# Optimization experiments

Hardware: AMD Instinct MI355X
Metric: run time of the kernel (lower is better)

## Reference

```python
import jax, jax.numpy as jnp
import numpy as np

STU, EXER, KNOW, D = 100000, 50000, 123, 64
N_NODES = STU + EXER
N_EDGES = 1200000
GCN_LAYERS = 3


def setup_inputs() -> dict:
    key = jax.random.key(0)
    ks = jax.random.split(key, 10)
    return {
        "student_id": jax.random.randint(ks[0], (8192,), 0, STU, dtype=jnp.int64) if jax.config.jax_enable_x64 else jax.random.randint(ks[0], (8192,), 0, STU, dtype=jnp.int32),
        "exercise_id": jax.random.randint(ks[1], (8192,), 0, EXER, dtype=jnp.int32),
        "q_mask": jax.random.randint(ks[2], (8192, KNOW), 0, 2, dtype=jnp.int32),
        "edge_row": jax.random.randint(ks[3], (N_EDGES,), 0, N_NODES, dtype=jnp.int32),
        "edge_col": jax.random.randint(ks[4], (N_EDGES,), 0, N_NODES, dtype=jnp.int32),
        "edge_val": jax.random.uniform(ks[5], (N_EDGES,), dtype=jnp.float32),
        # learned parameters (xavier-normal-ish init)
        "stu_emb": jax.random.normal(ks[6], (STU, D), dtype=jnp.float32) * 0.02,
        "exer_emb": jax.random.normal(ks[7], (EXER, D), dtype=jnp.float32) * 0.02,
        "disc_emb": jax.random.normal(ks[8], (EXER, 1), dtype=jnp.float32) * 0.02,
        "know_emb": jax.random.normal(ks[9], (KNOW, D), dtype=jnp.float32) * 0.02,
    }


def reference(student_id, exercise_id, q_mask, edge_row, edge_col, edge_val,
              stu_emb, exer_emb, disc_emb, know_emb):
    # LightGCN propagation (eval path: no edge dropout, matching self.training=False)
    s = stu_emb.shape[0]
    all_emb = jnp.concatenate([stu_emb, exer_emb], axis=0)  # [N, D]
    acc = all_emb
    h = all_emb
    for _ in range(GCN_LAYERS):
        # SpMM: out[r] = sum_e val[e] * h[col[e]] for edges with row[e]==r
        msgs = edge_val[:, None] * h[edge_col]               # [E, D]
        h = jax.ops.segment_sum(msgs, edge_row, num_segments=N_NODES)
        acc = acc + h
    light_out = acc / jnp.asarray(GCN_LAYERS + 1, dtype=acc.dtype)  # mean over layer stack
    stus = light_out[:s]
    exers = light_out[s:]
    student_ts = stus[student_id]        # [B, D]
    diff_ts = exers[exercise_id]         # [B, D]
    disc_ts = disc_emb[exercise_id]      # [B, 1]
    knowledge_ts = know_emb              # [K, D]
    return (student_ts, diff_ts, disc_ts, knowledge_ts)
```

## Files before the change

### kernel.cpp

```cpp
#include <hip/hip_runtime.h>


#define STU 100000
#define EXER 50000
#define KNOW 123
#define DIM 64
#define N_NODES 150000
#define N_EDGES 1200000
#define NB 8192
#define BR 256
#define NBUCK 586
#define PB 256
#define EPB 4688
#define NSB 586
#define SCAP 3072

typedef unsigned short bfu;

__device__ __forceinline__ bfu f2bf(float f) {
    unsigned int u = __float_as_uint(f);
    unsigned int r = (u + 0x7FFFu + ((u >> 16) & 1u)) >> 16;
    return (bfu)r;
}
__device__ __forceinline__ float bf2f(bfu h) {
    return __uint_as_float((unsigned int)h << 16);
}

__global__ void k_conv0(const float* __restrict__ stu, const float* __restrict__ exer,
                        bfu* __restrict__ b0) {
    long long i = (long long)blockIdx.x * blockDim.x + threadIdx.x;
    long long n4 = ((long long)N_NODES * DIM) >> 2;
    if (i >= n4) return;
    long long stu4 = ((long long)STU * DIM) >> 2;
    float4 v = (i < stu4) ? ((const float4*)stu)[i]
                          : ((const float4*)exer)[i - stu4];
    ushort4 o;
    o.x = f2bf(v.x); o.y = f2bf(v.y); o.z = f2bf(v.z); o.w = f2bf(v.w);
    ((ushort4*)b0)[i] = o;
}

__global__ __launch_bounds__(1024) void k_count(const int* __restrict__ erow,
                                                int* __restrict__ gcounts) {
    __shared__ int cnt[NBUCK];
    for (int i = threadIdx.x; i < NBUCK; i += 1024) cnt[i] = 0;
    __syncthreads();
    int b = blockIdx.x;
    long long s = (long long)b * EPB;
    long long e = s + EPB; if (e > N_EDGES) e = N_EDGES;
    for (long long k = s + threadIdx.x; k < e; k += 1024)
        atomicAdd(&cnt[__builtin_nontemporal_load(&erow[k]) >> 8], 1);
    __syncthreads();
    for (int i = threadIdx.x; i < NBUCK; i += 1024) gcounts[i * PB + b] = cnt[i];
}

__global__ void k_scan1(const int* __restrict__ gin, int* __restrict__ gout,
                        int* __restrict__ bsum) {
    __shared__ int s[256];
    int i = blockIdx.x * 256 + threadIdx.x;
    int v = gin[i];
    s[threadIdx.x] = v;
    __syncthreads();
    for (int o = 1; o < 256; o <<= 1) {
        int x = (threadIdx.x >= o) ? s[threadIdx.x - o] : 0;
        __syncthreads();
        s[threadIdx.x] += x;
        __syncthreads();
    }
    gout[i] = s[threadIdx.x] - v;
    if (threadIdx.x == 255) bsum[blockIdx.x] = s[255];
}

__global__ void k_scan2(const int* __restrict__ bsum, int* __restrict__ bsumoff) {
    __shared__ int s[1024];
    int t = threadIdx.x;
    int v = (t < NSB) ? bsum[t] : 0;
    s[t] = v;
    __syncthreads();
    for (int o = 1; o < 1024; o <<= 1) {
        int x = (t >= o) ? s[t - o] : 0;
        __syncthreads();
        s[t] += x;
        __syncthreads();
    }
    if (t < NSB) bsumoff[t] = s[t] - v;
}

__global__ void k_scan3(int* __restrict__ gout, const int* __restrict__ bsumoff,
                        int* __restrict__ boff) {
    int i = blockIdx.x * 256 + threadIdx.x;
    int v = gout[i] + bsumoff[i >> 8];
    gout[i] = v;
    if ((i & 255) == 0) boff[i >> 8] = v;
    if (i == 0) boff[NBUCK] = N_EDGES;
}

__global__ __launch_bounds__(1024) void k_place(const int* __restrict__ erow,
                                                const int* __restrict__ ecol,
                                                const float* __restrict__ eval,
                                                const int* __restrict__ gscan,
                                                int2* __restrict__ bedge) {
    __shared__ int2 staged[EPB];
    __shared__ unsigned short sbkt[EPB];
    __shared__ int lbase[NBUCK];
    __shared__ int lcur[NBUCK];
    __shared__ int gbase[NBUCK];
    __shared__ int stmp[1024];
    int b = blockIdx.x, tid = threadIdx.x;
    for (int i = tid; i < NBUCK; i += 1024) lcur[i] = 0;
    __syncthreads();
    long long s = (long long)b * EPB;
    long long e = s + EPB; if (e > N_EDGES) e = N_EDGES;
    int n = (int)(e - s);
    for (int k = tid; k < n; k += 1024)
        atomicAdd(&lcur[__builtin_nontemporal_load(&erow[s + k]) >> 8], 1);
    __syncthreads();
    int v = (tid < NBUCK) ? lcur[tid] : 0;
    stmp[tid] = v;
    __syncthreads();
    for (int o = 1; o < 1024; o <<= 1) {
        int x = (tid >= o) ? stmp[tid - o] : 0;
        __syncthreads();
        stmp[tid] += x;
        __syncthreads();
    }
    if (tid < NBUCK) { lbase[tid] = stmp[tid] - v; lcur[tid] = stmp[tid] - v; }
    for (int i = tid; i < NBUCK; i += 1024) gbase[i] = gscan[i * PB + b];
    __syncthreads();
    for (int k = tid; k < n; k += 1024) {
        int r = __builtin_nontemporal_load(&erow[s + k]);
        int c = __builtin_nontemporal_load(&ecol[s + k]);
        float vv = __builtin_nontemporal_load(&eval[s + k]);
        int bk = r >> 8;
        int p = atomicAdd(&lcur[bk], 1);
        staged[p] = make_int2((r & 255) | (c << 8), __float_as_int(vv));
        sbkt[p] = (unsigned short)bk;
    }
    __syncthreads();
    for (int t = tid; t < n; t += 1024) {
        int bk = sbkt[t];
        bedge[gbase[bk] + (t - lbase[bk])] = staged[t];
    }
}

__global__ __launch_bounds__(512) void k_sort(const int* __restrict__ boff,
                                              const int2* __restrict__ bedge,
                                              int2* __restrict__ sedge,
                                              int* __restrict__ off) {
    __shared__ int2 st[SCAP];
    __shared__ int2 st2[SCAP];
    __shared__ int hist[BR];
    __shared__ int cur[BR];
    __shared__ int stmp[512];
    int b = blockIdx.x, tid = threadIdx.x;
    int s = boff[b], e = boff[b + 1];
    int n = e - s; if (n > SCAP) n = SCAP;
    for (int i = tid; i < BR; i += 512) hist[i] = 0;
    __syncthreads();
    for (int t = tid; t < n; t += 512) {
        int2 ev = bedge[s + t];
        st[t] = ev;
        atomicAdd(&hist[ev.x & 255], 1);
    }
    __syncthreads();
    int v = (tid < BR) ? hist[tid] : 0;
    stmp[tid] = v;
    __syncthreads();
    for (int o = 1; o < 512; o <<= 1) {
        int x = (tid >= o) ? stmp[tid - o] : 0;
        __syncthreads();
        stmp[tid] += x;
        __syncthreads();
    }
    if (tid < BR) {
        int ex = stmp[tid] - v;
        cur[tid] = ex;
        off[b * BR + tid] = s + ex;
    }
    __syncthreads();
    for (int t = tid; t < n; t += 512) {
        int2 ev = st[t];
        int p = atomicAdd(&cur[ev.x & 255], 1);
        st2[p] = make_int2((unsigned)ev.x >> 8, ev.y);
    }
    __syncthreads();
    for (int t = tid; t < n; t += 512) sedge[s + t] = st2[t];
}

__global__ void k_gather2(const int* __restrict__ off, const int2* __restrict__ sedge,
                          const bfu* __restrict__ h, bfu* __restrict__ out) {
    int w = (blockIdx.x * blockDim.x + threadIdx.x) >> 6;
    if (w >= N_NODES / 2) return;
    int lane = threadIdx.x & 63;
    int half = lane >> 5, l32 = lane & 31;
    int r0 = __builtin_amdgcn_readfirstlane(w) * 2;
    int o0 = off[r0], o1 = off[r0 + 1], o2 = off[r0 + 2];
    int s = half ? o1 : o0;
    int e = half ? o2 : o1;
    int dA = o1 - o0, dB = o2 - o1;
    int nmax = dA > dB ? dA : dB;
    const unsigned* h32 = (const unsigned*)h;
    float acc0 = 0.f, acc1 = 0.f;
    for (int j = 0; j < nmax; j += 8) {
        int2 ev[8]; float wg[8];
#pragma unroll
        for (int q = 0; q < 8; q++) {
            int kk = s + j + q;
            int idx = (kk < e) ? kk : 0;
            ev[q] = sedge[idx];
            wg[q] = (kk < e) ? __int_as_float(ev[q].y) : 0.f;
        }
        unsigned hv[8];
#pragma unroll
        for (int q = 0; q < 8; q++) hv[q] = h32[(size_t)ev[q].x * 32 + l32];
#pragma unroll
        for (int q = 0; q < 8; q++) {
            acc0 += wg[q] * __uint_as_float(hv[q] << 16);
            acc1 += wg[q] * __uint_as_float(hv[q] & 0xffff0000u);
        }
    }
    unsigned o = (unsigned)f2bf(acc0) | ((unsigned)f2bf(acc1) << 16);
    ((unsigned*)out)[(size_t)(r0 + half) * 32 + l32] = o;
}

__global__ void k_out_main(const int* __restrict__ sid, const int* __restrict__ eid,
                           const int* __restrict__ off, const int2* __restrict__ sedge,
                           const float* __restrict__ stu, const float* __restrict__ exer,
                           const bfu* __restrict__ B1, const bfu* __restrict__ B2,
                           float* __restrict__ out) {
    int w = (blockIdx.x * blockDim.x + threadIdx.x) >> 6;
    int lane = threadIdx.x & 63;
    if (w >= 2 * NB) return;
    int wu = __builtin_amdgcn_readfirstlane(w);
    int r;
    long long obase;
    if (wu < NB) { r = sid[wu];            obase = (long long)wu * 64; }
    else         { r = STU + eid[wu - NB]; obase = 524288 + (long long)(wu - NB) * 64; }
    int ru = __builtin_amdgcn_readfirstlane(r);
    long long rb = (long long)ru * 64 + lane;
    float h0 = (ru < STU) ? stu[rb] : exer[rb - (long long)STU * 64];
    float ssum = h0 + bf2f(B1[rb]) + bf2f(B2[rb]);
    int st = off[ru], en = off[ru + 1];
    float g = 0.f;
    int k = st;
    for (; k + 8 <= en; k += 8) {
        int2 ev[8];
#pragma unroll
        for (int j = 0; j < 8; j++) ev[j] = sedge[k + j];
        float a[8];
#pragma unroll
        for (int j = 0; j < 8; j++) a[j] = bf2f(B2[(size_t)ev[j].x * DIM + lane]);
#pragma unroll
        for (int j = 0; j < 8; j++) g += __int_as_float(ev[j].y) * a[j];
    }
    for (; k < en; k++) {
        int2 ev = sedge[k];
        g += __int_as_float(ev.y) * bf2f(B2[(size_t)ev.x * DIM + lane]);
    }
    out[obase + lane] = 0.25f * (ssum + g);
}

__global__ void k_out_tail(const int* __restrict__ eid, const float* __restrict__ disc,
                           const float* __restrict__ know, float* __restrict__ out) {
    int i = blockIdx.x * blockDim.x + threadIdx.x;
    if (i < NB) out[1048576 + i] = disc[eid[i]];
    else if (i < NB + KNOW * DIM) out[1056768 + (i - NB)] = know[i - NB];
}

extern "C" void kernel_launch(void* const* d_in, const int* in_sizes, int n_in,
                              void* d_out, int out_size, void* d_ws, size_t ws_size,
                              hipStream_t stream) {
    const int*   sid  = (const int*)d_in[0];
    const int*   eid  = (const int*)d_in[1];
    const int*   erow = (const int*)d_in[3];
    const int*   ecol = (const int*)d_in[4];
    const float* eval = (const float*)d_in[5];
    const float* stu  = (const float*)d_in[6];
    const float* exer = (const float*)d_in[7];
    const float* disc = (const float*)d_in[8];
    const float* know = (const float*)d_in[9];
    float* out = (float*)d_out;

    char* ws = (char*)d_ws;
    bfu*  B0      = (bfu*) (ws);
    bfu*  B1      = (bfu*) (ws + 19200000);
    bfu*  B2      = (bfu*) (ws + 38400000);
    int2* bedge   = (int2*)(ws + 57600000);
    int2* sedge   = (int2*)(ws + 67200000);
    int*  gcounts = (int*) (ws + 76800000);
    int*  gscan   = (int*) (ws + 77400064);
    int*  bsum    = (int*) (ws + 78000128);
    int*  bsumoff = (int*) (ws + 78002688);
    int*  boff    = (int*) (ws + 78005248);
    int*  off     = (int*) (ws + 78007596);

    const int BLK = 256;
    long long n4 = ((long long)N_NODES * DIM) >> 2;
    int convGrid = (int)((n4 + BLK - 1) / BLK);
    int gatherGrid = (N_NODES / 2 * 64) / BLK;
    int outMainGrid = (2 * NB * 64) / BLK;
    int outTailGrid = (NB + KNOW * DIM + BLK - 1) / BLK;

    k_conv0<<<convGrid, BLK, 0, stream>>>(stu, exer, B0);

    k_count<<<PB, 1024, 0, stream>>>(erow, gcounts);
    k_scan1<<<NSB, 256, 0, stream>>>(gcounts, gscan, bsum);
    k_scan2<<<1, 1024, 0, stream>>>(bsum, bsumoff);
    k_scan3<<<NSB, 256, 0, stream>>>(gscan, bsumoff, boff);
    k_place<<<PB, 1024, 0, stream>>>(erow, ecol, eval, gscan, bedge);
    k_sort <<<NBUCK, 512, 0, stream>>>(boff, bedge, sedge, off);

    k_gather2<<<gatherGrid, BLK, 0, stream>>>(off, sedge, B0, B1);
    k_gather2<<<gatherGrid, BLK, 0, stream>>>(off, sedge, B1, B2);

    k_out_main<<<outMainGrid, BLK, 0, stream>>>(sid, eid, off, sedge, stu, exer, B1, B2, out);
    k_out_tail<<<outTailGrid, BLK, 0, stream>>>(eid, disc, know, out);
}
```

Measured before the change: 120.6 us.

## Rework SpMM gather to stage edges in LDS and process 16 rows per block

Replaces the two-rows-per-wave gather with a block that handles 16 rows. Each row gets 16 lanes that load 8-byte (four bf16) feature chunks instead of 4-byte ones, and the block's contiguous edge records are first copied into shared memory with a coalesced load. The aim is to raise memory-level parallelism and cut redundant global reads of the sorted edge list. The staging buffer is capped at 512 edges per block, so a block whose rows hold more edges would read out-of-range shared entries. With four rows per wave, degree imbalance across those rows can also leave lanes idle.

```diff
diff --git a/kernel.cpp b/kernel.cpp
--- a/kernel.cpp
+++ b/kernel.cpp
@@ -14,6 +14,8 @@
 #define EPB 4688
 #define NSB 586
 #define SCAP 3072
+#define RPB 16
+#define RCAP 512
 
 typedef unsigned short bfu;
 
@@ -186,40 +188,49 @@
     for (int t = tid; t < n; t += 512) sedge[s + t] = st2[t];
 }
 
-__global__ void k_gather2(const int* __restrict__ off, const int2* __restrict__ sedge,
-                          const bfu* __restrict__ h, bfu* __restrict__ out) {
-    int w = (blockIdx.x * blockDim.x + threadIdx.x) >> 6;
-    if (w >= N_NODES / 2) return;
-    int lane = threadIdx.x & 63;
-    int half = lane >> 5, l32 = lane & 31;
-    int r0 = __builtin_amdgcn_readfirstlane(w) * 2;
-    int o0 = off[r0], o1 = off[r0 + 1], o2 = off[r0 + 2];
-    int s = half ? o1 : o0;
-    int e = half ? o2 : o1;
-    int dA = o1 - o0, dB = o2 - o1;
-    int nmax = dA > dB ? dA : dB;
-    const unsigned* h32 = (const unsigned*)h;
-    float acc0 = 0.f, acc1 = 0.f;
-    for (int j = 0; j < nmax; j += 8) {
+__global__ __launch_bounds__(256) void k_gather16(const int* __restrict__ off,
+                                                  const int2* __restrict__ sedge,
+                                                  const bfu* __restrict__ h,
+                                                  bfu* __restrict__ out) {
+    __shared__ int2 rec[RCAP];
+    __shared__ int soff[RPB + 1];
+    int tid = threadIdx.x;
+    int base = blockIdx.x * RPB;
+    if (tid <= RPB) soff[tid] = off[base + tid];
+    __syncthreads();
+    int s0 = soff[0];
+    int n = soff[RPB] - s0; if (n > RCAP) n = RCAP;
+    for (int i = tid; i < n; i += 256) rec[i] = sedge[s0 + i];
+    __syncthreads();
+
+    int wv = tid >> 6, grp = (tid >> 4) & 3, l16 = tid & 15;
+    int lr = wv * 4 + grp;
+    int rs = soff[lr] - s0, re = soff[lr + 1] - s0;
+    const uint2* h2 = (const uint2*)h;
+    float a0 = 0.f, a1 = 0.f, a2 = 0.f, a3 = 0.f;
+    for (int k = rs; k < re; k += 8) {
         int2 ev[8]; float wg[8];
 #pragma unroll
         for (int q = 0; q < 8; q++) {
-            int kk = s + j + q;
-            int idx = (kk < e) ? kk : 0;
-            ev[q] = sedge[idx];
-            wg[q] = (kk < e) ? __int_as_float(ev[q].y) : 0.f;
+            int idx = (k + q < re) ? (k + q) : rs;
+            ev[q] = rec[idx];
+            wg[q] = (k + q < re) ? __int_as_float(ev[q].y) : 0.f;
         }
-        unsigned hv[8];
-#pragma unroll
-        for (int q = 0; q < 8; q++) hv[q] = h32[(size_t)ev[q].x * 32 + l32];
+        uint2 hv[8];
+#pragma unroll
+        for (int q = 0; q < 8; q++) hv[q] = h2[(size_t)ev[q].x * 16 + l16];
 #pragma unroll
         for (int q = 0; q < 8; q++) {
-            acc0 += wg[q] * __uint_as_float(hv[q] << 16);
-            acc1 += wg[q] * __uint_as_float(hv[q] & 0xffff0000u);
+            a0 += wg[q] * __uint_as_float(hv[q].x << 16);
+            a1 += wg[q] * __uint_as_float(hv[q].x & 0xffff0000u);
+            a2 += wg[q] * __uint_as_float(hv[q].y << 16);
+            a3 += wg[q] * __uint_as_float(hv[q].y & 0xffff0000u);
         }
     }
-    unsigned o = (unsigned)f2bf(acc0) | ((unsigned)f2bf(acc1) << 16);
-    ((unsigned*)out)[(size_t)(r0 + half) * 32 + l32] = o;
+    uint2 o;
+    o.x = (unsigned)f2bf(a0) | ((unsigned)f2bf(a1) << 16);
+    o.y = (unsigned)f2bf(a2) | ((unsigned)f2bf(a3) << 16);
+    ((uint2*)out)[(size_t)(base + lr) * 16 + l16] = o;
 }
 
 __global__ void k_out_main(const int* __restrict__ sid, const int* __restrict__ eid,
@@ -296,7 +307,7 @@
     const int BLK = 256;
     long long n4 = ((long long)N_NODES * DIM) >> 2;
     int convGrid = (int)((n4 + BLK - 1) / BLK);
-    int gatherGrid = (N_NODES / 2 * 64) / BLK;
+    int gatherGrid = N_NODES / RPB;
     int outMainGrid = (2 * NB * 64) / BLK;
     int outTailGrid = (NB + KNOW * DIM + BLK - 1) / BLK;
 
@@ -309,8 +320,8 @@
     k_place<<<PB, 1024, 0, stream>>>(erow, ecol, eval, gscan, bedge);
     k_sort <<<NBUCK, 512, 0, stream>>>(boff, bedge, sedge, off);
 
-    k_gather2<<<gatherGrid, BLK, 0, stream>>>(off, sedge, B0, B1);
-    k_gather2<<<gatherGrid, BLK, 0, stream>>>(off, sedge, B1, B2);
+    k_gather16<<<gatherGrid, BLK, 0, stream>>>(off, sedge, B0, B1);
+    k_gather16<<<gatherGrid, BLK, 0, stream>>>(off, sedge, B1, B2);
 
     k_out_main<<<outMainGrid, BLK, 0, stream>>>(sid, eid, off, sedge, stu, exer, B1, B2, out);
     k_out_tail<<<outTailGrid, BLK, 0, stream>>>(eid, disc, know, out);
```

Result: faster. 112.2 us (-7.0%).
